# Optimization experiments

Hardware: AMD Instinct MI355X
Metric: run time of the kernel (lower is better)

## Reference

```python
import jax, jax.numpy as jnp
import numpy as np

EPS = 1e-5  # BatchNorm eps


def _bn(x, g, b, axes):
    # training-mode batch norm over `axes`, channel dim broadcast via g/b shape
    m = jnp.mean(x, axis=axes, keepdims=True)
    v = jnp.var(x, axis=axes, keepdims=True)
    shape = [1] * x.ndim
    ch_axis = [a for a in range(x.ndim) if a not in axes][0]
    shape[ch_axis] = g.shape[0]
    return g.reshape(shape) * (x - m) * jax.lax.rsqrt(v + EPS) + b.reshape(shape)


def setup_inputs() -> dict:
    key = jax.random.key(0)
    ks = jax.random.split(key, 8)
    B, C, N = 16, 3, 2048

    def w(k_, fan_in, fan_out):
        return jax.random.normal(k_, (fan_in, fan_out), jnp.float32) * (1.0 / np.sqrt(fan_in))

    return {
        "pc": jax.random.normal(ks[0], (B, C, N), jnp.float32),
        "W1": w(ks[1], 6, 64), "g1": jnp.ones(64), "b1": jnp.zeros(64),
        "W2": w(ks[2], 64, 128), "g2": jnp.ones(128), "b2": jnp.zeros(128),
        "W3": w(ks[3], 128, 1024), "g3": jnp.ones(1024), "b3": jnp.zeros(1024),
        "Wf1": w(ks[4], 1024, 512), "gf1": jnp.ones(512), "bf1": jnp.zeros(512),
        "Wf2": w(ks[5], 512, 256), "gf2": jnp.ones(256), "bf2": jnp.zeros(256),
        "Wf3": jnp.zeros((256, 9), jnp.float32),           # zero-initialized per source
        "bf3": jnp.eye(3, dtype=jnp.float32).reshape(-1),  # identity bias per source
        "k": 20,
    }


def reference(pc, W1, g1, b1, W2, g2, b2, W3, g3, b3,
              Wf1, gf1, bf1, Wf2, gf2, bf2, Wf3, bf3, k):
    B, C, N = pc.shape
    # ---- KNN graph on coordinates (B x C x N) ----
    sq = jnp.sum(pc * pc, axis=1)                      # B,N
    inner = jnp.einsum('bcn,bcm->bnm', pc, pc)         # B,N,N
    negdist = 2.0 * inner - sq[:, :, None] - sq[:, None, :]
    _, idx = jax.lax.top_k(negdist, k)                 # B,N,k (includes self)
    # gather neighbor features: f (C,N), i (N,k) -> (C,N,k)
    topk = jax.vmap(lambda f, i: f[:, i])(pc, idx)     # B,C,N,k
    center = pc[:, :, :, None]
    edge = jnp.concatenate(
        [jnp.broadcast_to(center, topk.shape), topk - center], axis=1)  # B,2C,N,k

    # ---- edge conv (1x1 conv + BN + ReLU), pool=False ----
    h = jnp.einsum('bcnk,co->bonk', edge, W1)
    h = jax.nn.relu(_bn(h, g1, b1, (0, 2, 3)))         # B,64,N,k
    # ---- conv2 then max over k ----
    h = jnp.einsum('bcnk,co->bonk', h, W2)
    h = jax.nn.relu(_bn(h, g2, b2, (0, 2, 3)))         # B,128,N,k
    h = jnp.max(h, axis=-1)                            # B,128,N
    # ---- conv3 then max over N ----
    h = jnp.einsum('bcn,co->bon', h, W3)
    h = jax.nn.relu(_bn(h, g3, b3, (0, 2)))            # B,1024,N
    h = jnp.max(h, axis=-1)                            # B,1024
    # ---- FC stack ----
    h = jax.nn.relu(_bn(h @ Wf1, gf1, bf1, (0,)))      # B,512
    h = jax.nn.relu(_bn(h @ Wf2, gf2, bf2, (0,)))      # B,256
    h = h @ Wf3 + bf3                                  # B,9
    return h.reshape(B, 3, 3)
```

## Files before the change

kernel.cpp:

```cpp
#include <hip/hip_runtime.h>
#include <math.h>

#define Nn 2048

#define OFF_IDX    ((size_t)0)
#define OFF_P2MAX  (((size_t)4)  << 20)
#define OFF_P2MIN  (((size_t)13) << 20)
#define OFF_PS2    (((size_t)22) << 20)
#define OFF_PQ2    (((size_t)23) << 20)
#define OFF_STATS  (((size_t)24) << 20)
#define OFF_MOM    (OFF_STATS + 0)
#define OFF_A1C1   (OFF_STATS + 4096)
#define OFF_A2C2   (OFF_STATS + 8192)
#define OFF_S3SUM  (OFF_STATS + 12288)
#define OFF_S3SQ   (OFF_STATS + 20480)
#define OFF_P3MAX  (OFF_STATS + 28672)
#define OFF_P3MIN  (OFF_STATS + 94208)
#define OFF_R3     (OFF_STATS + 159744)
#define OFF_R4     (OFF_STATS + 225280)
#define OFF_R5     (OFF_STATS + 258048)
#define OFF_DOTS1  (OFF_STATS + 274432)
#define OFF_DOTS2  (OFF_STATS + 307200)
#define WS_NEEDED  (OFF_STATS + 323584)

typedef __attribute__((ext_vector_type(8))) short bf16x8;
typedef __attribute__((ext_vector_type(4))) float f32x4;

__device__ __forceinline__ unsigned fkey(float f){
  unsigned u = __float_as_uint(f);
  return (u & 0x80000000u) ? ~u : (u | 0x80000000u);
}
__device__ __forceinline__ float fdec(unsigned k){
  unsigned u = (k & 0x80000000u) ? (k & 0x7FFFFFFFu) : ~k;
  return __uint_as_float(u);
}
__device__ __forceinline__ short f2bf(float x){
  unsigned u = __float_as_uint(x);
  u += 0x7fffu + ((u >> 16) & 1u);
  return (short)(u >> 16);
}
__device__ __forceinline__ float bf2f(short v){
  return __uint_as_float(((unsigned)(unsigned short)v) << 16);
}
__device__ __forceinline__ float med3(float a, float b, float c){
  float d;
  asm("v_med3_f32 %0, %1, %2, %3" : "=v"(d) : "v"(a), "v"(b), "v"(c));
  return d;
}
__device__ __forceinline__ float ndist(float tQx, float tQy, float tQz, float Qw, float4 P){
  return fmaf(tQx, P.x, fmaf(tQy, P.y, fmaf(tQz, P.z, -Qw - P.w)));
}
__device__ __forceinline__ void insert20(float (&m)[20], float x){
  #pragma unroll
  for (int t = 0; t < 19; t++) m[t] = med3(m[t], m[t+1], x);
  m[19] = fmaxf(m[19], x);
}

__global__ __launch_bounds__(256) void k_init(char* __restrict__ ws){
  int i = blockIdx.x*256 + threadIdx.x;
  if (i < 7168) ((unsigned*)(ws + OFF_MOM))[i] = 0u;
  if (i < 16384){
    ((unsigned*)(ws + OFF_P3MAX))[i] = 0u;
    ((unsigned*)(ws + OFF_P3MIN))[i] = 0xFFFFFFFFu;
  }
  if (i < 12288) ((float*)(ws + OFF_DOTS1))[i] = 0.f;
}

__global__ __launch_bounds__(256) void k_knn(const float* __restrict__ pc,
                                             int* __restrict__ idxg,
                                             double* __restrict__ MOM){
  __shared__ float4 pts[Nn];
  __shared__ unsigned cnt[32];
  __shared__ float momS[27];
  const int tid = threadIdx.x;
  const int b = blockIdx.y;
  const int n0 = blockIdx.x*32;
  const float* pcb = pc + b*3*Nn;
  for (int i = tid; i < Nn; i += 256){
    float x = pcb[i], y = pcb[Nn+i], z = pcb[2*Nn+i];
    pts[i] = make_float4(x, y, z, x*x + y*y + z*z);
  }
  if (tid < 32) cnt[tid] = 0u;
  if (tid < 27) momS[tid] = 0.f;
  __syncthreads();

  const int ql = tid >> 3, c = tid & 7;
  const int n = n0 + ql;
  const float4 Q = pts[n];
  const float tQx = 2.f*Q.x, tQy = 2.f*Q.y, tQz = 2.f*Q.z;

  float v[20];
  #pragma unroll
  for (int t = 0; t < 20; t++) v[t] = -3.4e38f;
  #pragma unroll 1
  for (int i = 0; i < 256; i += 4){
    float4 P0 = pts[(i+0)*8 + c];
    float4 P1 = pts[(i+1)*8 + c];
    float4 P2 = pts[(i+2)*8 + c];
    float4 P3 = pts[(i+3)*8 + c];
    insert20(v, ndist(tQx, tQy, tQz, Q.w, P0));
    insert20(v, ndist(tQx, tQy, tQz, Q.w, P1));
    insert20(v, ndist(tQx, tQy, tQz, Q.w, P2));
    insert20(v, ndist(tQx, tQy, tQz, Q.w, P3));
  }

  #pragma unroll
  for (int stage = 4; stage >= 1; stage >>= 1){
    float w[20];
    #pragma unroll
    for (int t = 0; t < 20; t++) w[t] = __shfl_xor(v[t], stage);
    #pragma unroll
    for (int t = 0; t < 20; t++) insert20(v, w[t]);
  }
  const float th = v[0];

  int* myidx = &idxg[((size_t)((b<<11) + n))*20];
  #pragma unroll 1
  for (int i = 0; i < 256; i += 4){
    float4 P0 = pts[(i+0)*8 + c];
    float4 P1 = pts[(i+1)*8 + c];
    float4 P2 = pts[(i+2)*8 + c];
    float4 P3 = pts[(i+3)*8 + c];
    float nd0 = ndist(tQx, tQy, tQz, Q.w, P0);
    float nd1 = ndist(tQx, tQy, tQz, Q.w, P1);
    float nd2 = ndist(tQx, tQy, tQz, Q.w, P2);
    float nd3 = ndist(tQx, tQy, tQz, Q.w, P3);
    if (nd0 >= th){ unsigned p = atomicAdd(&cnt[ql], 1u); if (p < 20u) myidx[p] = (i+0)*8 + c; }
    if (nd1 >= th){ unsigned p = atomicAdd(&cnt[ql], 1u); if (p < 20u) myidx[p] = (i+1)*8 + c; }
    if (nd2 >= th){ unsigned p = atomicAdd(&cnt[ql], 1u); if (p < 20u) myidx[p] = (i+2)*8 + c; }
    if (nd3 >= th){ unsigned p = atomicAdd(&cnt[ql], 1u); if (p < 20u) myidx[p] = (i+3)*8 + c; }
  }
  __threadfence_block();
  __syncthreads();

  if (c == 0){
    unsigned have = cnt[ql]; if (have > 20u) have = 20u;
    for (unsigned p = have; p < 20u; ++p) myidx[p] = n;
  }
  __threadfence_block();
  __syncthreads();

  float s1[6] = {0,0,0,0,0,0};
  float s2[21] = {0,0,0,0,0,0,0,0,0,0,0,0,0,0,0,0,0,0,0,0,0};
  #pragma unroll 1
  for (int j = tid; j < 640; j += 256){
    int q = j/20, t = j - q*20;
    int m = idxg[((size_t)((b<<11) + n0 + q))*20 + t] & 2047;
    float4 P = pts[m];
    float4 Qq = pts[n0 + q];
    float e[6] = {Qq.x, Qq.y, Qq.z, P.x - Qq.x, P.y - Qq.y, P.z - Qq.z};
    int u = 0;
    #pragma unroll
    for (int a = 0; a < 6; a++){
      s1[a] += e[a];
      #pragma unroll
      for (int bq = a; bq < 6; bq++){ s2[u] += e[a]*e[bq]; u++; }
    }
  }
  #pragma unroll
  for (int a = 0; a < 6; a++)
    for (int off = 32; off > 0; off >>= 1) s1[a] += __shfl_xor(s1[a], off);
  #pragma unroll
  for (int u = 0; u < 21; u++)
    for (int off = 32; off > 0; off >>= 1) s2[u] += __shfl_xor(s2[u], off);
  if ((tid & 63) == 0){
    #pragma unroll
    for (int a = 0; a < 6; a++) atomicAdd(&momS[a], s1[a]);
    #pragma unroll
    for (int u = 0; u < 21; u++) atomicAdd(&momS[6+u], s2[u]);
  }
  __syncthreads();
  if (tid < 27) atomicAdd(&MOM[tid], (double)momS[tid]);
}

__global__ __launch_bounds__(64) void k_coef1(const double* __restrict__ MOM,
        const float* __restrict__ W1, const float* __restrict__ g1,
        const float* __restrict__ b1, float* __restrict__ A1C1){
  const int o = threadIdx.x;
  const double inv = 1.0/655360.0;
  double w[6]; double m = 0.0;
  #pragma unroll
  for (int c = 0; c < 6; c++){ w[c] = (double)W1[c*64+o]; m += w[c]*MOM[c]*inv; }
  double e2 = 0.0; int u = 0;
  #pragma unroll
  for (int c = 0; c < 6; c++){
    #pragma unroll
    for (int cp = c; cp < 6; cp++){
      double mm = MOM[6+u]*inv; u++;
      e2 += (c == cp) ? w[c]*w[c]*mm : 2.0*w[c]*w[cp]*mm;
    }
  }
  double var = e2 - m*m;
  double a = (double)g1[o] / sqrt(var + 1e-5);
  #pragma unroll
  for (int c = 0; c < 6; c++) A1C1[c*64+o] = (float)(a*w[c]);
  A1C1[384+o] = (float)((double)b1[o] - a*m);
}

__global__ __launch_bounds__(256) void k_conv12(const float* __restrict__ pc,
      const int* __restrict__ idxg, const float* __restrict__ A1C1,
      const float* __restrict__ W2,
      float* __restrict__ PS2, float* __restrict__ PQ2,
      short* __restrict__ P2MAX, short* __restrict__ P2MIN){
  __shared__ float es[6][512];
  __shared__ short h1s[512*64];
  __shared__ float w1s[448];
  __shared__ float ssum[128], ssq[128];
  const int tid = threadIdx.x;
  const int b = blockIdx.y;
  const int n0 = blockIdx.x*16;
  const float* pcb = pc + b*3*Nn;

  for (int i = tid; i < 448; i += 256) w1s[i] = A1C1[i];

  for (int s = tid; s < 512; s += 256){
    int nl = s >> 5, kk = s & 31;
    int n = n0 + nl;
    int kke = (kk < 20) ? kk : 0;
    int m = idxg[((size_t)((b<<11)+n))*20 + kke] & 2047;
    float cx = pcb[n],  cy = pcb[Nn+n],  cz = pcb[2*Nn+n];
    float px = pcb[m],  py = pcb[Nn+m],  pz = pcb[2*Nn+m];
    es[0][s] = cx;    es[1][s] = cy;    es[2][s] = cz;
    es[3][s] = px-cx; es[4][s] = py-cy; es[5][s] = pz-cz;
  }
  __syncthreads();

  for (int i = tid; i < 4096; i += 256){
    int s = i >> 3, oc = i & 7;
    bf16x8 hv;
    #pragma unroll
    for (int j = 0; j < 8; j++){
      int o = oc*8 + j;
      float acc = w1s[384 + o];
      #pragma unroll
      for (int c = 0; c < 6; c++) acc = fmaf(w1s[c*64 + o], es[c][s], acc);
      hv[j] = f2bf(fmaxf(acc, 0.f));
    }
    *(bf16x8*)&h1s[s*64 + ((oc ^ (s & 7)) << 3)] = hv;
  }
  __syncthreads();

  const int l = tid & 63, wv = tid >> 6;
  const int col = l & 15, kc = l >> 4;

  bf16x8 Bf[2][2];
  #pragma unroll
  for (int qt = 0; qt < 2; qt++){
    int q = wv*32 + qt*16 + col;
    #pragma unroll
    for (int ks = 0; ks < 2; ks++){
      int k0 = ks*32 + kc*8;
      #pragma unroll
      for (int j = 0; j < 8; j++) Bf[qt][ks][j] = f2bf(W2[(k0+j)*128 + q]);
    }
  }

  float smacc[2] = {0.f, 0.f}, sqacc[2] = {0.f, 0.f};
  const bool t1real = (kc == 0);

  #pragma unroll 1
  for (int g = 0; g < 16; g++){
    bf16x8 Af[2][2];
    #pragma unroll
    for (int t = 0; t < 2; t++){
      int row = g*32 + t*16 + col;
      #pragma unroll
      for (int ks = 0; ks < 2; ks++){
        int chunk = (ks*4 + kc) ^ (row & 7);
        Af[t][ks] = *(const bf16x8*)&h1s[row*64 + chunk*8];
      }
    }
    #pragma unroll
    for (int qt = 0; qt < 2; qt++){
      f32x4 a0 = {0.f,0.f,0.f,0.f}, a1 = {0.f,0.f,0.f,0.f};
      a0 = __builtin_amdgcn_mfma_f32_16x16x32_bf16(Af[0][0], Bf[qt][0], a0, 0,0,0);
      a0 = __builtin_amdgcn_mfma_f32_16x16x32_bf16(Af[0][1], Bf[qt][1], a0, 0,0,0);
      a1 = __builtin_amdgcn_mfma_f32_16x16x32_bf16(Af[1][0], Bf[qt][0], a1, 0,0,0);
      a1 = __builtin_amdgcn_mfma_f32_16x16x32_bf16(Af[1][1], Bf[qt][1], a1, 0,0,0);
      float mx = a0[0], mn = a0[0], sm = 0.f, sq = 0.f;
      #pragma unroll
      for (int r = 0; r < 4; r++){
        float v0 = a0[r], v1 = a1[r];
        mx = fmaxf(mx, fmaxf(v0, v1));
        mn = fminf(mn, fminf(v0, v1));
        sm += v0; sq += v0*v0;
      }
      if (t1real){
        #pragma unroll
        for (int r = 0; r < 4; r++){ float v1 = a1[r]; sm += v1; sq += v1*v1; }
      }
      smacc[qt] += sm; sqacc[qt] += sq;
      mx = fmaxf(mx, __shfl_xor(mx, 16)); mx = fmaxf(mx, __shfl_xor(mx, 32));
      mn = fminf(mn, __shfl_xor(mn, 16)); mn = fminf(mn, __shfl_xor(mn, 32));
      if (kc == 0){
        size_t base = ((size_t)(b*Nn + n0 + g))*128 + (size_t)(wv*32 + qt*16 + col);
        P2MAX[base] = f2bf(mx);
        P2MIN[base] = f2bf(mn);
      }
    }
  }
  #pragma unroll
  for (int qt = 0; qt < 2; qt++){
    smacc[qt] += __shfl_xor(smacc[qt], 16); smacc[qt] += __shfl_xor(smacc[qt], 32);
    sqacc[qt] += __shfl_xor(sqacc[qt], 16); sqacc[qt] += __shfl_xor(sqacc[qt], 32);
    if (kc == 0){
      ssum[wv*32 + qt*16 + col] = smacc[qt];
      ssq [wv*32 + qt*16 + col] = sqacc[qt];
    }
  }
  __syncthreads();
  if (tid < 128){
    int bid = b*128 + blockIdx.x;
    PS2[tid*2048 + bid] = ssum[tid];
    PQ2[tid*2048 + bid] = ssq[tid];
  }
}

__global__ __launch_bounds__(256) void k_coef2(const float* __restrict__ PS2,
        const float* __restrict__ PQ2, const float* __restrict__ g2,
        const float* __restrict__ b2, float* __restrict__ A2C2){
  __shared__ float sred[4], qred[4];
  const int p = blockIdx.x;
  const int tid = threadIdx.x;
  float s = 0.f, q = 0.f;
  for (int i = tid; i < 2048; i += 256){ s += PS2[p*2048 + i]; q += PQ2[p*2048 + i]; }
  #pragma unroll
  for (int off = 32; off > 0; off >>= 1){ s += __shfl_xor(s, off); q += __shfl_xor(q, off); }
  if ((tid & 63) == 0){ sred[tid >> 6] = s; qred[tid >> 6] = q; }
  __syncthreads();
  if (tid == 0){
    double sum = (double)sred[0] + sred[1] + sred[2] + sred[3];
    double sq  = (double)qred[0] + qred[1] + qred[2] + qred[3];
    double mean = sum * (1.0/655360.0);
    double var  = sq  * (1.0/655360.0) - mean*mean;
    double a = (double)g2[p] / sqrt(var + 1e-5);
    A2C2[p]     = (float)a;
    A2C2[128+p] = (float)((double)b2[p] - a*mean);
  }
}

__global__ __launch_bounds__(256) void k_conv3(const short* __restrict__ P2MAX,
      const short* __restrict__ P2MIN, const float* __restrict__ A2C2,
      const float* __restrict__ W3, double* __restrict__ S3SUM,
      double* __restrict__ S3SQ, unsigned* __restrict__ P3MAX,
      unsigned* __restrict__ P3MIN){
  __shared__ short As[128*128];
  __shared__ float a2[128], c2[128];
  const int tid = threadIdx.x;
  const int b = blockIdx.y;
  const int n0 = blockIdx.x*128;
  const int qh = blockIdx.z;
  if (tid < 128){ a2[tid] = A2C2[tid]; c2[tid] = A2C2[128+tid]; }
  __syncthreads();

  for (int idx = tid; idx < 2048; idx += 256){
    int s = idx >> 4, oc = idx & 15;
    size_t base = ((size_t)(b*Nn + n0 + s))*128 + (size_t)(oc*8);
    bf16x8 vmx = *(const bf16x8*)&P2MAX[base];
    bf16x8 vmn = *(const bf16x8*)&P2MIN[base];
    bf16x8 vv;
    #pragma unroll
    for (int j = 0; j < 8; j++){
      int o = oc*8 + j;
      float aa = a2[o];
      float vsel = bf2f((aa >= 0.f) ? vmx[j] : vmn[j]);
      vv[j] = f2bf(fmaxf(aa*vsel + c2[o], 0.f));
    }
    int chunk = oc ^ (s & 7);
    *(bf16x8*)&As[s*128 + chunk*8] = vv;
  }
  __syncthreads();

  const int l = tid & 63, wv = tid >> 6;
  const int col = l & 15, kc = l >> 4;

  #pragma unroll 1
  for (int pass = 0; pass < 2; ++pass){
    bf16x8 Bf[4][4];
    #pragma unroll
    for (int qt = 0; qt < 4; qt++){
      int q = qh*512 + wv*128 + pass*64 + qt*16 + col;
      #pragma unroll
      for (int ks = 0; ks < 4; ks++){
        int k0 = ks*32 + kc*8;
        #pragma unroll
        for (int j = 0; j < 8; j++)
          Bf[qt][ks][j] = f2bf(W3[(size_t)(k0+j)*1024 + q]);
      }
    }
    float smx[4], smn[4], ssm[4], ssqv[4];
    #pragma unroll
    for (int qt = 0; qt < 4; qt++){ smx[qt] = -3.4e38f; smn[qt] = 3.4e38f; ssm[qt] = 0.f; ssqv[qt] = 0.f; }

    #pragma unroll 1
    for (int st = 0; st < 8; ++st){
      bf16x8 Af[4];
      int row = st*16 + col;
      #pragma unroll
      for (int ks = 0; ks < 4; ks++){
        int chunk = (ks*4 + kc) ^ (row & 7);
        Af[ks] = *(const bf16x8*)&As[row*128 + chunk*8];
      }
      #pragma unroll
      for (int qt = 0; qt < 4; qt++){
        f32x4 acc = {0.f, 0.f, 0.f, 0.f};
        #pragma unroll
        for (int ks = 0; ks < 4; ks++)
          acc = __builtin_amdgcn_mfma_f32_16x16x32_bf16(Af[ks], Bf[qt][ks], acc, 0, 0, 0);
        #pragma unroll
        for (int r = 0; r < 4; r++){
          float vv = acc[r];
          smx[qt] = fmaxf(smx[qt], vv); smn[qt] = fminf(smn[qt], vv);
          ssm[qt] += vv; ssqv[qt] += vv*vv;
        }
      }
    }
    #pragma unroll
    for (int qt = 0; qt < 4; qt++){
      #pragma unroll
      for (int off = 16; off <= 32; off <<= 1){
        smx[qt] = fmaxf(smx[qt], __shfl_xor(smx[qt], off));
        smn[qt] = fminf(smn[qt], __shfl_xor(smn[qt], off));
        ssm[qt] += __shfl_xor(ssm[qt], off);
        ssqv[qt] += __shfl_xor(ssqv[qt], off);
      }
    }
    if (kc == 0){
      #pragma unroll
      for (int qt = 0; qt < 4; qt++){
        int q = qh*512 + wv*128 + pass*64 + qt*16 + col;
        atomicMax(&P3MAX[b*1024 + q], fkey(smx[qt]));
        atomicMin(&P3MIN[b*1024 + q], fkey(smn[qt]));
        atomicAdd(&S3SUM[q], (double)ssm[qt]);
        atomicAdd(&S3SQ[q],  (double)ssqv[qt]);
      }
    }
  }
}

__global__ __launch_bounds__(256) void k_bn3relu(const double* __restrict__ S3SUM,
      const double* __restrict__ S3SQ, const unsigned* __restrict__ P3MAX,
      const unsigned* __restrict__ P3MIN, const float* __restrict__ g3,
      const float* __restrict__ b3, float* __restrict__ R3){
  int id = blockIdx.x*256 + threadIdx.x;
  int q = id & 1023;
  double mean = S3SUM[q] * (1.0/32768.0);
  double var  = S3SQ[q] * (1.0/32768.0) - mean*mean;
  double a = (double)g3[q] / sqrt(var + 1e-5);
  double c = (double)b3[q] - a*mean;
  float v = fdec((a >= 0.0) ? P3MAX[id] : P3MIN[id]);
  R3[id] = fmaxf((float)(a*(double)v + c), 0.f);
}

template<int IN, int OUT>
__global__ __launch_bounds__(256) void k_fcdot(const float* __restrict__ X,
      const float* __restrict__ W, float* __restrict__ dots){
  constexpr int L = IN/16;
  __shared__ float Xs[16*L];
  const int tid = threadIdx.x;
  const int o = blockIdx.x*64 + (tid & 63);
  const int wv = tid >> 6;
  const int c0 = blockIdx.y*L;
  for (int i = tid; i < 16*L; i += 256){
    int bb = i / L, cc = i - bb*L;
    Xs[i] = X[bb*IN + c0 + cc];
  }
  __syncthreads();
  constexpr int CPW = L/4;
  float acc[16];
  #pragma unroll
  for (int bb = 0; bb < 16; bb++) acc[bb] = 0.f;
  for (int cc = wv*CPW; cc < (wv+1)*CPW; ++cc){
    float w = W[(size_t)(c0+cc)*OUT + o];
    #pragma unroll
    for (int bb = 0; bb < 16; bb++) acc[bb] += Xs[bb*L + cc]*w;
  }
  #pragma unroll
  for (int bb = 0; bb < 16; bb++) atomicAdd(&dots[bb*OUT + o], acc[bb]);
}

template<int OUT>
__global__ __launch_bounds__(64) void k_fcbn(const float* __restrict__ dots,
      const float* __restrict__ g, const float* __restrict__ bet,
      float* __restrict__ Y){
  const int o = blockIdx.x*64 + threadIdx.x;
  float d[16]; float m = 0.f;
  #pragma unroll
  for (int bb = 0; bb < 16; bb++){ d[bb] = dots[bb*OUT + o]; m += d[bb]; }
  m *= (1.f/16.f);
  float v = 0.f;
  #pragma unroll
  for (int bb = 0; bb < 16; bb++){ float x = d[bb]-m; v += x*x; }
  v *= (1.f/16.f);
  float a = g[o] * rsqrtf(v + 1e-5f);
  #pragma unroll
  for (int bb = 0; bb < 16; bb++) Y[bb*OUT + o] = fmaxf(a*(d[bb]-m) + bet[o], 0.f);
}

__global__ __launch_bounds__(192) void k_head(const float* __restrict__ R5,
      const float* __restrict__ Wf3, const float* __restrict__ bf3,
      float* __restrict__ out){
  int t = threadIdx.x;
  if (t >= 144) return;
  int b = t/9, j = t - b*9;
  float acc = bf3[j];
  for (int c = 0; c < 256; c++) acc += R5[b*256 + c]*Wf3[c*9 + j];
  out[t] = acc;
}

extern "C" void kernel_launch(void* const* d_in, const int* in_sizes, int n_in,
                              void* d_out, int out_size, void* d_ws, size_t ws_size,
                              hipStream_t stream) {
  if (ws_size < WS_NEEDED) return;
  const float* pc  = (const float*)d_in[0];
  const float* W1  = (const float*)d_in[1];
  const float* g1  = (const float*)d_in[2];
  const float* b1  = (const float*)d_in[3];
  const float* W2  = (const float*)d_in[4];
  const float* g2  = (const float*)d_in[5];
  const float* b2  = (const float*)d_in[6];
  const float* W3  = (const float*)d_in[7];
  const float* g3  = (const float*)d_in[8];
  const float* b3  = (const float*)d_in[9];
  const float* Wf1 = (const float*)d_in[10];
  const float* gf1 = (const float*)d_in[11];
  const float* bf1 = (const float*)d_in[12];
  const float* Wf2 = (const float*)d_in[13];
  const float* gf2 = (const float*)d_in[14];
  const float* bf2 = (const float*)d_in[15];
  const float* Wf3 = (const float*)d_in[16];
  const float* bf3 = (const float*)d_in[17];

  char* ws = (char*)d_ws;
  int*      IDX   = (int*)     (ws + OFF_IDX);
  short*    P2MAXp= (short*)   (ws + OFF_P2MAX);
  short*    P2MINp= (short*)   (ws + OFF_P2MIN);
  float*    PS2p  = (float*)   (ws + OFF_PS2);
  float*    PQ2p  = (float*)   (ws + OFF_PQ2);
  double*   MOMp  = (double*)  (ws + OFF_MOM);
  float*    A1C1p = (float*)   (ws + OFF_A1C1);
  float*    A2C2p = (float*)   (ws + OFF_A2C2);
  double*   S3SUMp= (double*)  (ws + OFF_S3SUM);
  double*   S3SQp = (double*)  (ws + OFF_S3SQ);
  unsigned* P3MAXp= (unsigned*)(ws + OFF_P3MAX);
  unsigned* P3MINp= (unsigned*)(ws + OFF_P3MIN);
  float*    R3p   = (float*)   (ws + OFF_R3);
  float*    R4p   = (float*)   (ws + OFF_R4);
  float*    R5p   = (float*)   (ws + OFF_R5);
  float*    DOTS1p= (float*)   (ws + OFF_DOTS1);
  float*    DOTS2p= (float*)   (ws + OFF_DOTS2);

  k_init          <<<dim3(64),       256, 0, stream>>>(ws);
  k_knn           <<<dim3(64,16),    256, 0, stream>>>(pc, IDX, MOMp);
  k_coef1         <<<dim3(1),         64, 0, stream>>>(MOMp, W1, g1, b1, A1C1p);
  k_conv12        <<<dim3(128,16),   256, 0, stream>>>(pc, IDX, A1C1p, W2, PS2p, PQ2p, P2MAXp, P2MINp);
  k_coef2         <<<dim3(128),      256, 0, stream>>>(PS2p, PQ2p, g2, b2, A2C2p);
  k_conv3         <<<dim3(16,16,2),  256, 0, stream>>>(P2MAXp, P2MINp, A2C2p, W3, S3SUMp, S3SQp, P3MAXp, P3MINp);
  k_bn3relu       <<<dim3(64),       256, 0, stream>>>(S3SUMp, S3SQp, P3MAXp, P3MINp, g3, b3, R3p);
  k_fcdot<1024,512><<<dim3(8,16),    256, 0, stream>>>(R3p, Wf1, DOTS1p);
  k_fcbn<512>     <<<dim3(8),         64, 0, stream>>>(DOTS1p, gf1, bf1, R4p);
  k_fcdot<512,256><<<dim3(4,16),     256, 0, stream>>>(R4p, Wf2, DOTS2p);
  k_fcbn<256>     <<<dim3(4),         64, 0, stream>>>(DOTS2p, gf2, bf2, R5p);
  k_head          <<<dim3(1),        192, 0, stream>>>(R5p, Wf3, bf3, (float*)d_out);
}
```

Before: 236.3 us.

## Pre-cast W2/W3 to bf16 in a separate kernel and enlarge KNN blocks

```diff
diff --git a/kernel.cpp b/kernel.cpp
--- a/kernel.cpp
+++ b/kernel.cpp
@@ -21,7 +21,9 @@
 #define OFF_R5     (OFF_STATS + 258048)
 #define OFF_DOTS1  (OFF_STATS + 274432)
 #define OFF_DOTS2  (OFF_STATS + 307200)
-#define WS_NEEDED  (OFF_STATS + 323584)
+#define OFF_W2BF   (OFF_STATS + 323584)
+#define OFF_W3BF   (OFF_STATS + 339968)
+#define WS_NEEDED  (OFF_STATS + 602112)
 
 typedef __attribute__((ext_vector_type(8))) short bf16x8;
 typedef __attribute__((ext_vector_type(4))) float f32x4;
@@ -66,21 +68,41 @@
   if (i < 12288) ((float*)(ws + OFF_DOTS1))[i] = 0.f;
 }
 
-__global__ __launch_bounds__(256) void k_knn(const float* __restrict__ pc,
+__global__ __launch_bounds__(256) void k_castw(const float* __restrict__ W2,
+      const float* __restrict__ W3, short* __restrict__ W2BF,
+      short* __restrict__ W3BF){
+  int id = blockIdx.x*256 + threadIdx.x;
+  if (id < 16384){
+    int q = id >> 4, k0 = (id & 15)*8;
+    bf16x8 vv;
+    #pragma unroll
+    for (int j = 0; j < 8; j++) vv[j] = f2bf(W3[(size_t)(k0+j)*1024 + q]);
+    *(bf16x8*)&W3BF[q*128 + k0] = vv;
+  } else if (id < 17408){
+    int id2 = id - 16384;
+    int q = id2 >> 3, k0 = (id2 & 7)*8;
+    bf16x8 vv;
+    #pragma unroll
+    for (int j = 0; j < 8; j++) vv[j] = f2bf(W2[(k0+j)*128 + q]);
+    *(bf16x8*)&W2BF[q*64 + k0] = vv;
+  }
+}
+
+__global__ __launch_bounds__(512) void k_knn(const float* __restrict__ pc,
                                              int* __restrict__ idxg,
                                              double* __restrict__ MOM){
   __shared__ float4 pts[Nn];
-  __shared__ unsigned cnt[32];
+  __shared__ unsigned cnt[64];
   __shared__ float momS[27];
   const int tid = threadIdx.x;
   const int b = blockIdx.y;
-  const int n0 = blockIdx.x*32;
+  const int n0 = blockIdx.x*64;
   const float* pcb = pc + b*3*Nn;
-  for (int i = tid; i < Nn; i += 256){
+  for (int i = tid; i < Nn; i += 512){
     float x = pcb[i], y = pcb[Nn+i], z = pcb[2*Nn+i];
     pts[i] = make_float4(x, y, z, x*x + y*y + z*z);
   }
-  if (tid < 32) cnt[tid] = 0u;
+  if (tid < 64) cnt[tid] = 0u;
   if (tid < 27) momS[tid] = 0.f;
   __syncthreads();
 
@@ -143,7 +165,7 @@
   float s1[6] = {0,0,0,0,0,0};
   float s2[21] = {0,0,0,0,0,0,0,0,0,0,0,0,0,0,0,0,0,0,0,0,0};
   #pragma unroll 1
-  for (int j = tid; j < 640; j += 256){
+  for (int j = tid; j < 1280; j += 512){
     int q = j/20, t = j - q*20;
     int m = idxg[((size_t)((b<<11) + n0 + q))*20 + t] & 2047;
     float4 P = pts[m];
@@ -199,7 +221,7 @@
 
 __global__ __launch_bounds__(256) void k_conv12(const float* __restrict__ pc,
       const int* __restrict__ idxg, const float* __restrict__ A1C1,
-      const float* __restrict__ W2,
+      const short* __restrict__ W2BF,
       float* __restrict__ PS2, float* __restrict__ PQ2,
       short* __restrict__ P2MAX, short* __restrict__ P2MIN){
   __shared__ float es[6][512];
@@ -248,11 +270,8 @@
   for (int qt = 0; qt < 2; qt++){
     int q = wv*32 + qt*16 + col;
     #pragma unroll
-    for (int ks = 0; ks < 2; ks++){
-      int k0 = ks*32 + kc*8;
-      #pragma unroll
-      for (int j = 0; j < 8; j++) Bf[qt][ks][j] = f2bf(W2[(k0+j)*128 + q]);
-    }
+    for (int ks = 0; ks < 2; ks++)
+      Bf[qt][ks] = *(const bf16x8*)&W2BF[q*64 + ks*32 + kc*8];
   }
 
   float smacc[2] = {0.f, 0.f}, sqacc[2] = {0.f, 0.f};
@@ -341,7 +360,7 @@
 
 __global__ __launch_bounds__(256) void k_conv3(const short* __restrict__ P2MAX,
       const short* __restrict__ P2MIN, const float* __restrict__ A2C2,
-      const float* __restrict__ W3, double* __restrict__ S3SUM,
+      const short* __restrict__ W3BF, double* __restrict__ S3SUM,
       double* __restrict__ S3SQ, unsigned* __restrict__ P3MAX,
       unsigned* __restrict__ P3MIN){
   __shared__ short As[128*128];
@@ -381,12 +400,8 @@
     for (int qt = 0; qt < 4; qt++){
       int q = qh*512 + wv*128 + pass*64 + qt*16 + col;
       #pragma unroll
-      for (int ks = 0; ks < 4; ks++){
-        int k0 = ks*32 + kc*8;
-        #pragma unroll
-        for (int j = 0; j < 8; j++)
-          Bf[qt][ks][j] = f2bf(W3[(size_t)(k0+j)*1024 + q]);
-      }
+      for (int ks = 0; ks < 4; ks++)
+        Bf[qt][ks] = *(const bf16x8*)&W3BF[q*128 + ks*32 + kc*8];
     }
     float smx[4], smn[4], ssm[4], ssqv[4];
     #pragma unroll
@@ -549,13 +564,16 @@
   float*    R5p   = (float*)   (ws + OFF_R5);
   float*    DOTS1p= (float*)   (ws + OFF_DOTS1);
   float*    DOTS2p= (float*)   (ws + OFF_DOTS2);
+  short*    W2BFp = (short*)   (ws + OFF_W2BF);
+  short*    W3BFp = (short*)   (ws + OFF_W3BF);
 
   k_init          <<<dim3(64),       256, 0, stream>>>(ws);
-  k_knn           <<<dim3(64,16),    256, 0, stream>>>(pc, IDX, MOMp);
+  k_castw         <<<dim3(68),       256, 0, stream>>>(W2, W3, W2BFp, W3BFp);
+  k_knn           <<<dim3(32,16),    512, 0, stream>>>(pc, IDX, MOMp);
   k_coef1         <<<dim3(1),         64, 0, stream>>>(MOMp, W1, g1, b1, A1C1p);
-  k_conv12        <<<dim3(128,16),   256, 0, stream>>>(pc, IDX, A1C1p, W2, PS2p, PQ2p, P2MAXp, P2MINp);
+  k_conv12        <<<dim3(128,16),   256, 0, stream>>>(pc, IDX, A1C1p, W2BFp, PS2p, PQ2p, P2MAXp, P2MINp);
   k_coef2         <<<dim3(128),      256, 0, stream>>>(PS2p, PQ2p, g2, b2, A2C2p);
-  k_conv3         <<<dim3(16,16,2),  256, 0, stream>>>(P2MAXp, P2MINp, A2C2p, W3, S3SUMp, S3SQp, P3MAXp, P3MINp);
+  k_conv3         <<<dim3(16,16,2),  256, 0, stream>>>(P2MAXp, P2MINp, A2C2p, W3BFp, S3SUMp, S3SQp, P3MAXp, P3MINp);
   k_bn3relu       <<<dim3(64),       256, 0, stream>>>(S3SUMp, S3SQp, P3MAXp, P3MINp, g3, b3, R3p);
   k_fcdot<1024,512><<<dim3(8,16),    256, 0, stream>>>(R3p, Wf1, DOTS1p);
   k_fcbn<512>     <<<dim3(8),         64, 0, stream>>>(DOTS1p, gf1, bf1, R4p);
```

Result: no change. 238.0 us (+0.7%).
